# Kernel tuning notes

Hardware: AMD Instinct MI355X
Metric: run time of the kernel (lower is better)

## Reference

```python
import jax, jax.numpy as jnp
import numpy as np

N_NODES = 100000
N_EDGES = 1600000
D_IN = 128
D_OUT = 128


def setup_inputs() -> dict:
    key = jax.random.key(0)
    k1, k2, k3, k4 = jax.random.split(key, 4)
    x = jax.random.normal(k1, (N_NODES, D_IN), dtype=jnp.float32)
    # Xavier-uniform-like init for weight (exact distribution irrelevant for correctness baseline)
    weight = jax.random.normal(k2, (D_IN, D_OUT), dtype=jnp.float32) * (1.0 / np.sqrt(D_IN))
    bias = jnp.zeros((D_OUT,), dtype=jnp.float32)
    edge_index = jax.random.randint(k3, (2, N_EDGES), 0, N_NODES, dtype=jnp.int64 if jax.config.read('jax_enable_x64') else jnp.int32)
    edge_weight = jax.random.uniform(k4, (N_EDGES,), dtype=jnp.float32)
    return {"x": x, "weight": weight, "bias": bias,
            "edge_index": edge_index, "edge_weight": edge_weight}


def reference(x, weight, bias, edge_index, edge_weight):
    # support = X @ W   -- dense projection [N, D_out]
    support = x @ weight
    # output = A @ support -- SpMM via gather + weighted segment-sum
    src = edge_index[1]  # column index of adj (neighbor being aggregated)
    dst = edge_index[0]  # row index of adj (node receiving the message)
    messages = support[src] * edge_weight[:, None]          # [E, D_out]
    out = jax.ops.segment_sum(messages, dst, num_segments=N_NODES)  # [N, D_out]
    return out + bias
```

## Files before the change

kernel.cpp:

```cpp
#include <hip/hip_runtime.h>
#include <hip/hip_bf16.h>

#define N_NODES 100000
#define N_EDGES 1600000
#define D 128

#define BSH 6
#define NBUK 1563
#define CAP 1344
#define NSCAT 256
#define PA_EPB 6250
#define NGB ((N_NODES / 16 + 15) / 16)
#define SRC_MASK 0x03FFFFFF

typedef __attribute__((ext_vector_type(8))) short bf16x8;
typedef __attribute__((ext_vector_type(4))) float f32x4;

static __device__ __forceinline__ short f2bf(float f) {
    unsigned u = __builtin_bit_cast(unsigned, f);
    u += 0x7FFFu + ((u >> 16) & 1u);
    return (short)(u >> 16);
}
static __device__ __forceinline__ float bf2f(unsigned short h) {
    unsigned u = ((unsigned)h) << 16;
    return __builtin_bit_cast(float, u);
}

__global__ void wt_kernel(const float* __restrict__ w, short* __restrict__ wt,
                          int* __restrict__ gcur) {
    const int i = blockIdx.x * blockDim.x + threadIdx.x;
    if (i < D * D) {
        const int k = i / D, c = i % D;
        wt[c * D + k] = f2bf(w[i]);
    }
    if (i < NBUK) gcur[i] = 0;
}

__global__ __launch_bounds__(1024, 8) void gemm_scatter_kernel(
    const float* __restrict__ x, const short* __restrict__ wt,
    short* __restrict__ sup, const int* __restrict__ dst,
    const int* __restrict__ src, const float* __restrict__ ew,
    int* __restrict__ gcur, int2* __restrict__ inter_sw) {
    __shared__ int h[NBUK];
    const int t = threadIdx.x;

    if (blockIdx.x < NSCAT) {
        for (int j = t; j < NBUK; j += 1024) h[j] = 0;
        __syncthreads();
        const int beg = blockIdx.x * PA_EPB;
        const int end = min(beg + PA_EPB, N_EDGES);
        for (int i = beg + t; i < end; i += 1024)
            atomicAdd(&h[dst[i] >> BSH], 1);
        __syncthreads();
        for (int j = t; j < NBUK; j += 1024) {
            const int c = h[j];
            h[j] = c ? (j * CAP + atomicAdd(&gcur[j], c)) : 0;
        }
        __syncthreads();
        for (int i = beg + t; i < end; i += 1024) {
            const int d = dst[i];
            const int pos = atomicAdd(&h[d >> BSH], 1);
            inter_sw[pos] = make_int2(src[i] | ((d & 63) << 26),
                                      __float_as_int(ew[i]));
        }
        return;
    }

    const int wid = (blockIdx.x - NSCAT) * 16 + (t >> 6);
    if (wid >= N_NODES / 16) return;
    const int l = t & 63;
    const int r = l & 15, g = l >> 4;
    const size_t row0 = (size_t)wid * 16;

    bf16x8 a[4];
    const float* xp = x + (row0 + r) * D + g * 8;
#pragma unroll
    for (int ks = 0; ks < 4; ++ks) {
        const float4 f0 = *reinterpret_cast<const float4*>(xp + ks * 32);
        const float4 f1 = *reinterpret_cast<const float4*>(xp + ks * 32 + 4);
        bf16x8 tt;
        tt[0] = f2bf(f0.x); tt[1] = f2bf(f0.y); tt[2] = f2bf(f0.z); tt[3] = f2bf(f0.w);
        tt[4] = f2bf(f1.x); tt[5] = f2bf(f1.y); tt[6] = f2bf(f1.z); tt[7] = f2bf(f1.w);
        a[ks] = tt;
    }

#pragma unroll
    for (int nt = 0; nt < 8; ++nt) {
        f32x4 acc = {0.f, 0.f, 0.f, 0.f};
        const short* wp = wt + (size_t)(nt * 16 + r) * D + g * 8;
#pragma unroll
        for (int ks = 0; ks < 4; ++ks) {
            const bf16x8 b = *reinterpret_cast<const bf16x8*>(wp + ks * 32);
            acc = __builtin_amdgcn_mfma_f32_16x16x32_bf16(a[ks], b, acc, 0, 0, 0);
        }
        short* sp = sup + (row0 + g * 4) * D + nt * 16 + r;
#pragma unroll
        for (int q = 0; q < 4; ++q) sp[q * D] = f2bf(acc[q]);
    }
}

__global__ __launch_bounds__(512) void sortagg_kernel(
    const int* __restrict__ gcur, const int2* __restrict__ inter_sw,
    const short* __restrict__ sup, const float* __restrict__ bias,
    float* __restrict__ out) {
    __shared__ int2 eb[CAP];
    __shared__ int st[64];
    __shared__ int cur[64];
    const int b = blockIdx.x, t = threadIdx.x;
    const int cnt = gcur[b];
    const int2* in = inter_sw + (size_t)b * CAP;

    if (t < 64) st[t] = 0;
    __syncthreads();

    int2 e0, e1, e2;
    const int i0 = t, i1 = t + 512, i2 = t + 1024;
    if (i0 < cnt) { e0 = in[i0]; atomicAdd(&st[(unsigned)e0.x >> 26], 1); }
    if (i1 < cnt) { e1 = in[i1]; atomicAdd(&st[(unsigned)e1.x >> 26], 1); }
    if (i2 < cnt) { e2 = in[i2]; atomicAdd(&st[(unsigned)e2.x >> 26], 1); }
    __syncthreads();

    if (t < 64) {
        const int hv = st[t];
        int s = hv;
#pragma unroll
        for (int o = 1; o < 64; o <<= 1) {
            const int v = __shfl_up(s, o);
            if (t >= o) s += v;
        }
        st[t] = s - hv;
        cur[t] = s - hv;
    }
    __syncthreads();

    if (i0 < cnt) eb[atomicAdd(&cur[(unsigned)e0.x >> 26], 1)] = make_int2(e0.x & SRC_MASK, e0.y);
    if (i1 < cnt) eb[atomicAdd(&cur[(unsigned)e1.x >> 26], 1)] = make_int2(e1.x & SRC_MASK, e1.y);
    if (i2 < cnt) eb[atomicAdd(&cur[(unsigned)e2.x >> 26], 1)] = make_int2(e2.x & SRC_MASK, e2.y);
    __syncthreads();

    const int wv = t >> 6, lane = t & 63;
    const int g = lane >> 4;
    const int fl = lane & 15;

    const float4 b0 = *reinterpret_cast<const float4*>(&bias[fl * 8]);
    const float4 b1 = *reinterpret_cast<const float4*>(&bias[fl * 8 + 4]);

    for (int k = 0; k < 8; ++k) {
        const int nl = wv * 8 + k;
        const int node = (b << BSH) + nl;
        if (node >= N_NODES) break;
        const int beg = st[nl], end = cur[nl];

        float acc[8] = {0, 0, 0, 0, 0, 0, 0, 0};
        for (int i = beg + g; i < end; i += 4) {
            const int2 sw = eb[i];
            const float w = __int_as_float(sw.y);
            const bf16x8 v = *reinterpret_cast<const bf16x8*>(
                &sup[(size_t)sw.x * D + fl * 8]);
#pragma unroll
            for (int q = 0; q < 8; ++q)
                acc[q] = fmaf(w, bf2f((unsigned short)v[q]), acc[q]);
        }
#pragma unroll
        for (int q = 0; q < 8; ++q) {
            acc[q] += __shfl_xor(acc[q], 16);
            acc[q] += __shfl_xor(acc[q], 32);
        }
        if (g == 0) {
            float* o = &out[(size_t)node * D + fl * 8];
            reinterpret_cast<float4*>(o)[0] =
                make_float4(acc[0] + b0.x, acc[1] + b0.y, acc[2] + b0.z, acc[3] + b0.w);
            reinterpret_cast<float4*>(o)[1] =
                make_float4(acc[4] + b1.x, acc[5] + b1.y, acc[6] + b1.z, acc[7] + b1.w);
        }
    }
}

extern "C" void kernel_launch(void* const* d_in, const int* in_sizes, int n_in,
                              void* d_out, int out_size, void* d_ws, size_t ws_size,
                              hipStream_t stream) {
    const float* x      = (const float*)d_in[0];
    const float* weight = (const float*)d_in[1];
    const float* bias   = (const float*)d_in[2];
    const int*   eidx   = (const int*)d_in[3];
    const float* ew     = (const float*)d_in[4];
    float* out = (float*)d_out;

    const int* dst_idx = eidx;
    const int* src_idx = eidx + N_EDGES;

    char* p = (char*)d_ws;
    short* sup       = (short*)p;  p += (size_t)N_NODES * D * 2;
    short* wt        = (short*)p;  p += (size_t)D * D * 2;
    int*   gcur      = (int*)p;    p += ((NBUK * 4 + 15) / 16) * 16;
    int2*  inter_sw  = (int2*)p;   p += (size_t)NBUK * CAP * 8;

    wt_kernel<<<(D * D + 255) / 256, 256, 0, stream>>>(weight, wt, gcur);

    gemm_scatter_kernel<<<NSCAT + NGB, 1024, 0, stream>>>(
        x, wt, sup, dst_idx, src_idx, ew, gcur, inter_sw);

    sortagg_kernel<<<NBUK, 512, 0, stream>>>(gcur, inter_sw, sup, bias, out);
}
```

Measured before the change: 133.1 us.

## Use 128-node scatter buckets split across two aggregation blocks

Switches the edge-bucketing to 128-node buckets (782 used, 1024 allocated) so the scatter phase needs fewer global counters and a single-pass histogram per thread. Each aggregation block now reads a whole 128-node bucket but keeps only the half matching its 64 nodes, so the bucket data is read twice. This cuts global atomic contention and per-bucket padding in the scatter, at the cost of doubling intermediate reads in the aggregation. It also adds a risk that a bucket overflows its 2560-entry capacity.

```diff
diff --git a/kernel.cpp b/kernel.cpp
--- a/kernel.cpp
+++ b/kernel.cpp
@@ -5,13 +5,15 @@
 #define N_EDGES 1600000
 #define D 128
 
-#define BSH 6
-#define NBUK 1563
-#define CAP 1344
+#define NBUK 1024
+#define BSH 7
+#define CAP 2560
+#define CAP_H 1344
+#define NAGG2 (((N_NODES + 127) >> BSH) * 2)
 #define NSCAT 256
 #define PA_EPB 6250
 #define NGB ((N_NODES / 16 + 15) / 16)
-#define SRC_MASK 0x03FFFFFF
+#define SRC_MASK 0x01FFFFFF
 
 typedef __attribute__((ext_vector_type(8))) short bf16x8;
 typedef __attribute__((ext_vector_type(4))) float f32x4;
@@ -45,22 +47,22 @@
     const int t = threadIdx.x;
 
     if (blockIdx.x < NSCAT) {
-        for (int j = t; j < NBUK; j += 1024) h[j] = 0;
+        if (t < NBUK) h[t] = 0;
         __syncthreads();
         const int beg = blockIdx.x * PA_EPB;
         const int end = min(beg + PA_EPB, N_EDGES);
         for (int i = beg + t; i < end; i += 1024)
             atomicAdd(&h[dst[i] >> BSH], 1);
         __syncthreads();
-        for (int j = t; j < NBUK; j += 1024) {
-            const int c = h[j];
-            h[j] = c ? (j * CAP + atomicAdd(&gcur[j], c)) : 0;
+        if (t < NBUK) {
+            const int c = h[t];
+            h[t] = c ? (t * CAP + atomicAdd(&gcur[t], c)) : 0;
         }
         __syncthreads();
         for (int i = beg + t; i < end; i += 1024) {
             const int d = dst[i];
             const int pos = atomicAdd(&h[d >> BSH], 1);
-            inter_sw[pos] = make_int2(src[i] | ((d & 63) << 26),
+            inter_sw[pos] = make_int2(src[i] | ((d & 127) << 25),
                                       __float_as_int(ew[i]));
         }
         return;
@@ -103,21 +105,25 @@
     const int* __restrict__ gcur, const int2* __restrict__ inter_sw,
     const short* __restrict__ sup, const float* __restrict__ bias,
     float* __restrict__ out) {
-    __shared__ int2 eb[CAP];
+    __shared__ int2 eb[CAP_H];
     __shared__ int st[64];
     __shared__ int cur[64];
     const int b = blockIdx.x, t = threadIdx.x;
-    const int cnt = gcur[b];
-    const int2* in = inter_sw + (size_t)b * CAP;
+    const int cb = b >> 1, hf = b & 1;
+    const int cnt = gcur[cb];
+    const int2* in = inter_sw + (size_t)cb * CAP;
 
     if (t < 64) st[t] = 0;
     __syncthreads();
 
-    int2 e0, e1, e2;
-    const int i0 = t, i1 = t + 512, i2 = t + 1024;
-    if (i0 < cnt) { e0 = in[i0]; atomicAdd(&st[(unsigned)e0.x >> 26], 1); }
-    if (i1 < cnt) { e1 = in[i1]; atomicAdd(&st[(unsigned)e1.x >> 26], 1); }
-    if (i2 < cnt) { e2 = in[i2]; atomicAdd(&st[(unsigned)e2.x >> 26], 1); }
+    int2 e0, e1, e2, e3, e4;
+    bool k0 = false, k1 = false, k2 = false, k3 = false, k4 = false;
+    const int i0 = t, i1 = t + 512, i2 = t + 1024, i3 = t + 1536, i4 = t + 2048;
+    if (i0 < cnt) { e0 = in[i0]; const int d7 = (unsigned)e0.x >> 25; if ((d7 >> 6) == hf) { k0 = true; atomicAdd(&st[d7 & 63], 1); } }
+    if (i1 < cnt) { e1 = in[i1]; const int d7 = (unsigned)e1.x >> 25; if ((d7 >> 6) == hf) { k1 = true; atomicAdd(&st[d7 & 63], 1); } }
+    if (i2 < cnt) { e2 = in[i2]; const int d7 = (unsigned)e2.x >> 25; if ((d7 >> 6) == hf) { k2 = true; atomicAdd(&st[d7 & 63], 1); } }
+    if (i3 < cnt) { e3 = in[i3]; const int d7 = (unsigned)e3.x >> 25; if ((d7 >> 6) == hf) { k3 = true; atomicAdd(&st[d7 & 63], 1); } }
+    if (i4 < cnt) { e4 = in[i4]; const int d7 = (unsigned)e4.x >> 25; if ((d7 >> 6) == hf) { k4 = true; atomicAdd(&st[d7 & 63], 1); } }
     __syncthreads();
 
     if (t < 64) {
@@ -133,21 +139,24 @@
     }
     __syncthreads();
 
-    if (i0 < cnt) eb[atomicAdd(&cur[(unsigned)e0.x >> 26], 1)] = make_int2(e0.x & SRC_MASK, e0.y);
-    if (i1 < cnt) eb[atomicAdd(&cur[(unsigned)e1.x >> 26], 1)] = make_int2(e1.x & SRC_MASK, e1.y);
-    if (i2 < cnt) eb[atomicAdd(&cur[(unsigned)e2.x >> 26], 1)] = make_int2(e2.x & SRC_MASK, e2.y);
+    if (k0) eb[atomicAdd(&cur[((unsigned)e0.x >> 25) & 63], 1)] = make_int2(e0.x & SRC_MASK, e0.y);
+    if (k1) eb[atomicAdd(&cur[((unsigned)e1.x >> 25) & 63], 1)] = make_int2(e1.x & SRC_MASK, e1.y);
+    if (k2) eb[atomicAdd(&cur[((unsigned)e2.x >> 25) & 63], 1)] = make_int2(e2.x & SRC_MASK, e2.y);
+    if (k3) eb[atomicAdd(&cur[((unsigned)e3.x >> 25) & 63], 1)] = make_int2(e3.x & SRC_MASK, e3.y);
+    if (k4) eb[atomicAdd(&cur[((unsigned)e4.x >> 25) & 63], 1)] = make_int2(e4.x & SRC_MASK, e4.y);
     __syncthreads();
 
     const int wv = t >> 6, lane = t & 63;
     const int g = lane >> 4;
     const int fl = lane & 15;
+    const int node0 = (cb << BSH) + (hf << 6);
 
     const float4 b0 = *reinterpret_cast<const float4*>(&bias[fl * 8]);
     const float4 b1 = *reinterpret_cast<const float4*>(&bias[fl * 8 + 4]);
 
     for (int k = 0; k < 8; ++k) {
         const int nl = wv * 8 + k;
-        const int node = (b << BSH) + nl;
+        const int node = node0 + nl;
         if (node >= N_NODES) break;
         const int beg = st[nl], end = cur[nl];
 
@@ -192,7 +201,7 @@
     char* p = (char*)d_ws;
     short* sup       = (short*)p;  p += (size_t)N_NODES * D * 2;
     short* wt        = (short*)p;  p += (size_t)D * D * 2;
-    int*   gcur      = (int*)p;    p += ((NBUK * 4 + 15) / 16) * 16;
+    int*   gcur      = (int*)p;    p += NBUK * 4;
     int2*  inter_sw  = (int2*)p;   p += (size_t)NBUK * CAP * 8;
 
     wt_kernel<<<(D * D + 255) / 256, 256, 0, stream>>>(weight, wt, gcur);
@@ -200,5 +209,5 @@
     gemm_scatter_kernel<<<NSCAT + NGB, 1024, 0, stream>>>(
         x, wt, sup, dst_idx, src_idx, ew, gcur, inter_sw);
 
-    sortagg_kernel<<<NBUK, 512, 0, stream>>>(gcur, inter_sw, sup, bias, out);
-}
+    sortagg_kernel<<<NAGG2, 512, 0, stream>>>(gcur, inter_sw, sup, bias, out);
+}
```

New measurement: 130.6 us. About the same (-1.9%).

## Split fused GEMM/scatter kernel into separate scatter and MFMA GEMM launches

Applied to the files above, without the earlier changes.

The combined kernel that ran edge bucketing and the bf16 MFMA projection in different blocks of one launch is split into two kernels. The scatter now uses twice as many blocks, each handling half as many edges, and the GEMM runs as 256-thread blocks without the 1024-thread occupancy constraint. This is meant to improve load balance and occupancy for each phase, at the cost of an extra launch and no longer overlapping the two phases.

```diff
diff --git a/kernel.cpp b/kernel.cpp
--- a/kernel.cpp
+++ b/kernel.cpp
@@ -8,9 +8,8 @@
 #define BSH 6
 #define NBUK 1563
 #define CAP 1344
-#define NSCAT 256
-#define PA_EPB 6250
-#define NGB ((N_NODES / 16 + 15) / 16)
+#define NSCAT 512
+#define PA_EPB 3125
 #define SRC_MASK 0x03FFFFFF
 
 typedef __attribute__((ext_vector_type(8))) short bf16x8;
@@ -36,39 +35,12 @@
     if (i < NBUK) gcur[i] = 0;
 }
 
-__global__ __launch_bounds__(1024, 8) void gemm_scatter_kernel(
+__global__ __launch_bounds__(256) void gemm_mfma_kernel(
     const float* __restrict__ x, const short* __restrict__ wt,
-    short* __restrict__ sup, const int* __restrict__ dst,
-    const int* __restrict__ src, const float* __restrict__ ew,
-    int* __restrict__ gcur, int2* __restrict__ inter_sw) {
-    __shared__ int h[NBUK];
-    const int t = threadIdx.x;
-
-    if (blockIdx.x < NSCAT) {
-        for (int j = t; j < NBUK; j += 1024) h[j] = 0;
-        __syncthreads();
-        const int beg = blockIdx.x * PA_EPB;
-        const int end = min(beg + PA_EPB, N_EDGES);
-        for (int i = beg + t; i < end; i += 1024)
-            atomicAdd(&h[dst[i] >> BSH], 1);
-        __syncthreads();
-        for (int j = t; j < NBUK; j += 1024) {
-            const int c = h[j];
-            h[j] = c ? (j * CAP + atomicAdd(&gcur[j], c)) : 0;
-        }
-        __syncthreads();
-        for (int i = beg + t; i < end; i += 1024) {
-            const int d = dst[i];
-            const int pos = atomicAdd(&h[d >> BSH], 1);
-            inter_sw[pos] = make_int2(src[i] | ((d & 63) << 26),
-                                      __float_as_int(ew[i]));
-        }
-        return;
-    }
-
-    const int wid = (blockIdx.x - NSCAT) * 16 + (t >> 6);
+    short* __restrict__ sup) {
+    const int wid = blockIdx.x * 4 + (threadIdx.x >> 6);
     if (wid >= N_NODES / 16) return;
-    const int l = t & 63;
+    const int l = threadIdx.x & 63;
     const int r = l & 15, g = l >> 4;
     const size_t row0 = (size_t)wid * 16;
 
@@ -78,10 +50,10 @@
     for (int ks = 0; ks < 4; ++ks) {
         const float4 f0 = *reinterpret_cast<const float4*>(xp + ks * 32);
         const float4 f1 = *reinterpret_cast<const float4*>(xp + ks * 32 + 4);
-        bf16x8 tt;
-        tt[0] = f2bf(f0.x); tt[1] = f2bf(f0.y); tt[2] = f2bf(f0.z); tt[3] = f2bf(f0.w);
-        tt[4] = f2bf(f1.x); tt[5] = f2bf(f1.y); tt[6] = f2bf(f1.z); tt[7] = f2bf(f1.w);
-        a[ks] = tt;
+        bf16x8 t;
+        t[0] = f2bf(f0.x); t[1] = f2bf(f0.y); t[2] = f2bf(f0.z); t[3] = f2bf(f0.w);
+        t[4] = f2bf(f1.x); t[5] = f2bf(f1.y); t[6] = f2bf(f1.z); t[7] = f2bf(f1.w);
+        a[ks] = t;
     }
 
 #pragma unroll
@@ -96,6 +68,32 @@
         short* sp = sup + (row0 + g * 4) * D + nt * 16 + r;
 #pragma unroll
         for (int q = 0; q < 4; ++q) sp[q * D] = f2bf(acc[q]);
+    }
+}
+
+__global__ __launch_bounds__(1024) void bukscatter_kernel(
+    const int* __restrict__ dst, const int* __restrict__ src,
+    const float* __restrict__ ew, int* __restrict__ gcur,
+    int2* __restrict__ inter_sw) {
+    __shared__ int h[NBUK];
+    const int t = threadIdx.x;
+    for (int j = t; j < NBUK; j += 1024) h[j] = 0;
+    __syncthreads();
+    const int beg = blockIdx.x * PA_EPB;
+    const int end = min(beg + PA_EPB, N_EDGES);
+    for (int i = beg + t; i < end; i += 1024)
+        atomicAdd(&h[dst[i] >> BSH], 1);
+    __syncthreads();
+    for (int j = t; j < NBUK; j += 1024) {
+        const int c = h[j];
+        h[j] = c ? (j * CAP + atomicAdd(&gcur[j], c)) : 0;
+    }
+    __syncthreads();
+    for (int i = beg + t; i < end; i += 1024) {
+        const int d = dst[i];
+        const int pos = atomicAdd(&h[d >> BSH], 1);
+        inter_sw[pos] = make_int2(src[i] | ((d & 63) << 26),
+                                  __float_as_int(ew[i]));
     }
 }
 
@@ -141,13 +139,14 @@
     const int wv = t >> 6, lane = t & 63;
     const int g = lane >> 4;
     const int fl = lane & 15;
+    const int node0 = b << BSH;
 
     const float4 b0 = *reinterpret_cast<const float4*>(&bias[fl * 8]);
     const float4 b1 = *reinterpret_cast<const float4*>(&bias[fl * 8 + 4]);
 
     for (int k = 0; k < 8; ++k) {
         const int nl = wv * 8 + k;
-        const int node = (b << BSH) + nl;
+        const int node = node0 + nl;
         if (node >= N_NODES) break;
         const int beg = st[nl], end = cur[nl];
 
@@ -197,8 +196,10 @@
 
     wt_kernel<<<(D * D + 255) / 256, 256, 0, stream>>>(weight, wt, gcur);
 
-    gemm_scatter_kernel<<<NSCAT + NGB, 1024, 0, stream>>>(
-        x, wt, sup, dst_idx, src_idx, ew, gcur, inter_sw);
+    bukscatter_kernel<<<NSCAT, 1024, 0, stream>>>(dst_idx, src_idx, ew, gcur,
+                                                  inter_sw);
+
+    gemm_mfma_kernel<<<(N_NODES / 16 + 3) / 4, 256, 0, stream>>>(x, wt, sup);
 
     sortagg_kernel<<<NBUK, 512, 0, stream>>>(gcur, inter_sw, sup, bias, out);
 }
```

After: 142.4 us. 1.07x slower.
